# Kernel optimization log

Measured on AMD Instinct MI355X. Metric: run time of the kernel, lower is better.

Reference implementation:

```python
import jax, jax.numpy as jnp
import numpy as np

BUCKETS = 256


def _gru_cell(x, h, W_ih, W_hh, b_ih, b_hh):
    # torch GRUCell math, gate order (r, z, n)
    gi = x @ W_ih.T + b_ih            # [B, 3H]
    gh = h @ W_hh.T + b_hh            # [B, 3H]
    i_r, i_z, i_n = jnp.split(gi, 3, axis=-1)
    h_r, h_z, h_n = jnp.split(gh, 3, axis=-1)
    r = jax.nn.sigmoid(i_r + h_r)
    z = jax.nn.sigmoid(i_z + h_z)
    n = jnp.tanh(i_n + r * h_n)
    return (1.0 - z) * n + z * h


def setup_inputs() -> dict:
    key = jax.random.key(0)
    ks = jax.random.split(key, 10)
    B, T, C, G, H, V = 16, 2000, 128, 512, 512, BUCKETS
    s = 0.1  # keep gates in a sane range
    return {
        "cond": jax.random.normal(ks[0], (B, T, C), jnp.float32),
        "h0": jnp.zeros((B, G), jnp.float32),
        "W_ih": jax.random.normal(ks[1], (3 * G, C), jnp.float32) * s,
        "W_hh": jax.random.normal(ks[2], (3 * G, G), jnp.float32) * s,
        "b_ih": jax.random.normal(ks[3], (3 * G,), jnp.float32) * s,
        "b_hh": jax.random.normal(ks[4], (3 * G,), jnp.float32) * s,
        "W_hid": jax.random.normal(ks[5], (H, G), jnp.float32) * s,
        "b_hid": jax.random.normal(ks[6], (H,), jnp.float32) * s,
        "W_out": jax.random.normal(ks[7], (V, H), jnp.float32) * s,
        "b_out": jax.random.normal(ks[8], (V,), jnp.float32) * s,
        "embedding": jax.random.normal(ks[9], (V, C), jnp.float32) * s,
    }


def reference(cond, h0, W_ih, W_hh, b_ih, b_hh, W_hid, b_hid, W_out, b_out, embedding):
    B, T, C = cond.shape
    keys = jax.random.split(jax.random.key(1), T)
    prev0 = jnp.full((B,), BUCKETS // 2, jnp.int32)  # mid-bucket = mu-law zero

    def step(carry, inp):
        h, prev = carry
        cond_t, k = inp
        x = cond_t + embedding[prev]                  # [B, C]
        h = _gru_cell(x, h, W_ih, W_hh, b_ih, b_hh)   # [B, G]
        hid = jax.nn.relu(h @ W_hid.T + b_hid)        # [B, H]
        logits = hid @ W_out.T + b_out                # [B, V]
        sample = jax.random.categorical(k, logits, axis=-1).astype(jnp.int32)
        return (h, sample), (logits, sample)

    (h_final, _), (logits, samples) = jax.lax.scan(
        step, (h0, prev0), (jnp.swapaxes(cond, 0, 1), keys))
    # logits: [T, B, V] -> [B, T, V]; samples: [T, B] -> [B, T]
    return jnp.swapaxes(logits, 0, 1), jnp.swapaxes(samples, 0, 1), h_final
```

## Files before the change

### kernel.cpp

```cpp
#include <hip/hip_runtime.h>
#include <stdint.h>
#include <math.h>

#define NBLK 128
#define NTHR 256
#define Bn 16
#define Tn 2000
#define Cn 128
#define Gn 512
#define Hn 512
#define Vn 256

#define WS_DBL_BASE 512
#define GRP_STRIDE  3072

#define OUT_SAMP ((size_t)Bn*Tn*Vn)
#define OUT_HF   (OUT_SAMP + (size_t)Bn*Tn)

typedef __attribute__((ext_vector_type(2))) double d2_t;

__device__ __forceinline__ unsigned rotl32(unsigned v, int n) {
  return (v << n) | (v >> (32 - n));
}

__device__ __forceinline__ void threefry2x32(unsigned k0, unsigned k1,
                                             unsigned c0, unsigned c1,
                                             unsigned& o0, unsigned& o1) {
  unsigned ks2 = k0 ^ k1 ^ 0x1BD11BDAu;
  unsigned x0 = c0 + k0;
  unsigned x1 = c1 + k1;
#define TF_R(r) { x0 += x1; x1 = rotl32(x1, r); x1 ^= x0; }
  TF_R(13) TF_R(15) TF_R(26) TF_R(6)
  x0 += k1;  x1 += ks2 + 1u;
  TF_R(17) TF_R(29) TF_R(16) TF_R(24)
  x0 += ks2; x1 += k0 + 2u;
  TF_R(13) TF_R(15) TF_R(26) TF_R(6)
  x0 += k0;  x1 += k1 + 3u;
  TF_R(17) TF_R(29) TF_R(16) TF_R(24)
  x0 += k1;  x1 += ks2 + 4u;
  TF_R(13) TF_R(15) TF_R(26) TF_R(6)
  x0 += ks2; x1 += k0 + 5u;
#undef TF_R
  o0 = x0; o1 = x1;
}

__device__ __forceinline__ double jax_gumbel(unsigned kt0, unsigned kt1,
                                             unsigned f) {
  unsigned r0, r1;
  threefry2x32(kt0, kt1, 0u, f, r0, r1);
  unsigned bits = r0 ^ r1;
  float uf = __uint_as_float((bits >> 9) | 0x3f800000u) - 1.0f;
  if (uf <= 0.f) uf = 1.17549435e-38f;
  return -log(-log((double)uf));
}

__device__ __forceinline__ void st_d(double* p, double v) {
  asm volatile("global_store_dwordx2 %0, %1, off sc0 sc1"
               :: "v"(p), "v"(v) : "memory");
}
__device__ __forceinline__ d2_t ld_d2(const double* p) {
  d2_t r;
  asm volatile("global_load_dwordx4 %0, %1, off sc0 sc1\n\t"
               "s_waitcnt vmcnt(0)" : "=&v"(r) : "v"(p));
  return r;
}
__device__ __forceinline__ void ld8(const double* pl, int v, double* o) {
  const double* a0 = pl + v;
  const double* a1 = pl + 512 + v;
  const double* a2 = pl + 1024 + v;
  const double* a3 = pl + 1536 + v;
  double o0, o1, o2, o3, o4, o5, o6, o7;
  asm volatile(
    "global_load_dwordx2 %[r0], %[p0], off sc0 sc1\n\t"
    "global_load_dwordx2 %[r1], %[p0], off offset:2048 sc0 sc1\n\t"
    "global_load_dwordx2 %[r2], %[p1], off sc0 sc1\n\t"
    "global_load_dwordx2 %[r3], %[p1], off offset:2048 sc0 sc1\n\t"
    "global_load_dwordx2 %[r4], %[p2], off sc0 sc1\n\t"
    "global_load_dwordx2 %[r5], %[p2], off offset:2048 sc0 sc1\n\t"
    "global_load_dwordx2 %[r6], %[p3], off sc0 sc1\n\t"
    "global_load_dwordx2 %[r7], %[p3], off offset:2048 sc0 sc1\n\t"
    "s_waitcnt vmcnt(0)"
    : [r0]"=&v"(o0), [r1]"=&v"(o1), [r2]"=&v"(o2), [r3]"=&v"(o3),
      [r4]"=&v"(o4), [r5]"=&v"(o5), [r6]"=&v"(o6), [r7]"=&v"(o7)
    : [p0]"v"(a0), [p1]"v"(a1), [p2]"v"(a2), [p3]"v"(a3));
  o[0]=o0; o[1]=o1; o[2]=o2; o[3]=o3; o[4]=o4; o[5]=o5; o[6]=o6; o[7]=o7;
}
__device__ __forceinline__ unsigned ld_u(const unsigned* p) {
  unsigned r;
  asm volatile("global_load_dword %0, %1, off sc0 sc1\n\t"
               "s_waitcnt vmcnt(0)" : "=&v"(r) : "v"(p) : "memory");
  return r;
}

__device__ __forceinline__ void gar(unsigned* ctr) {
  asm volatile("s_waitcnt vmcnt(0)" ::: "memory");
  __syncthreads();
  if (threadIdx.x == 0) atomicAdd(ctr, 1u);
}
__device__ __forceinline__ void gwt(unsigned* ctr, unsigned target) {
  if (threadIdx.x == 0) {
    int guard = 0;
    while (ld_u(ctr) < target) {
      if (++guard > 5000000) break;
    }
  }
  asm volatile("" ::: "memory");
  __syncthreads();
}

extern "C" __global__ __launch_bounds__(NTHR)
void wavernn_pipe(const float* __restrict__ cond, const float* __restrict__ h0,
                  const float* __restrict__ W_ih, const float* __restrict__ W_hh,
                  const float* __restrict__ b_ih, const float* __restrict__ b_hh,
                  const float* __restrict__ W_hid, const float* __restrict__ b_hid,
                  const float* __restrict__ W_out, const float* __restrict__ b_out,
                  const float* __restrict__ emb,
                  float* __restrict__ out, double* __restrict__ ws) {
  const int tid = threadIdx.x;
  const int blk = blockIdx.x;
  const int g = blk >> 3;
  const int j = blk & 7;
  const int lane = tid & 63, wv = tid >> 6;

  unsigned* ctrH = ((unsigned*)ws) + (size_t)g * 64;
  unsigned* ctrP = ((unsigned*)ws) + (size_t)g * 64 + 32;
  double* G   = ws + WS_DBL_BASE + (size_t)g * GRP_STRIDE;
  double* Hb0 = G;
  double* Hb1 = G + 512;
  double* PL  = G + 1024;

  __shared__ __attribute__((aligned(32))) double s_x[Cn];
  __shared__ __attribute__((aligned(32))) double s_h[Gn];
  __shared__ __attribute__((aligned(32))) double s_hid[64];
  __shared__ double s_hn[64], s_in[64], s_z[64];
  __shared__ double s_part[4][64];
  __shared__ double s_gum[256];
  __shared__ float  s_cond[Cn];
  __shared__ double s_pv[4];
  __shared__ int    s_pi[4];

  if (tid < 64) st_d(&Hb0[j * 64 + tid],
                     (double)h0[(size_t)g * Gn + j * 64 + tid]);
  if (tid < Cn) s_x[tid] = (double)cond[(size_t)g * Tn * Cn + tid]
                         + (double)emb[128 * Cn + tid];
  gar(ctrH); gwt(ctrH, 8u);
  ((d2_t*)s_h)[tid] = ld_d2(Hb0 + 2 * tid);
  __syncthreads();

  for (int t = 0; t < Tn; ++t) {
    double* hnxt = (t & 1) ? Hb0 : Hb1;

    double ha0 = 0., ha1 = 0., ha2 = 0., ha3 = 0.;
    if (wv <= 2) {
      const int row = wv * 512 + j * 64 + lane;
      const float4* wh = (const float4*)(W_hh + (size_t)row * Gn);
      const double4* h4 = (const double4*)s_h;
#pragma unroll 8
      for (int k = 0; k < Gn / 4; ++k) {
        float4 w = wh[k]; double4 hv = h4[k];
        ha0 = fma((double)w.x, hv.x, ha0); ha1 = fma((double)w.y, hv.y, ha1);
        ha2 = fma((double)w.z, hv.z, ha2); ha3 = fma((double)w.w, hv.w, ha3);
      }
      if (wv == 2)
        s_hn[lane] = ((ha0 + ha1) + (ha2 + ha3)) + (double)b_hh[row];
    } else {
      const int c0 = 2 * lane;
      s_cond[c0]     = cond[((size_t)g * Tn + t) * Cn + c0];
      s_cond[c0 + 1] = cond[((size_t)g * Tn + t) * Cn + c0 + 1];
      if (t > 0) {
        unsigned kt0, kt1;
        threefry2x32(0u, 1u, 0u, (unsigned)(t - 1), kt0, kt1);
#pragma unroll
        for (int i = 0; i < 4; ++i) {
          int v = 4 * lane + i;
          s_gum[v] = jax_gumbel(kt0, kt1, (unsigned)(g * Vn + v));
        }
      }
    }

    if (t > 0) {
      gwt(ctrP, (unsigned)(8 * t));
      const int v = tid;
      double l[8];
      ld8(PL, v, l);
      double logit = ((((((((l[0] + l[1]) + l[2]) + l[3]) + l[4]) + l[5])
                       + l[6]) + l[7])) + (double)b_out[v];
      if (j == 0)
        out[(size_t)g * Tn * Vn + (size_t)(t - 1) * Vn + v] = (float)logit;
      double bv = logit + s_gum[v];
      int bi = v;
#pragma unroll
      for (int off = 1; off < 64; off <<= 1) {
        double ov = __shfl_xor(bv, off, 64);
        int oi = __shfl_xor(bi, off, 64);
        if (ov > bv || (ov == bv && oi < bi)) { bv = ov; bi = oi; }
      }
      if (lane == 0) { s_pv[wv] = bv; s_pi[wv] = bi; }
      __syncthreads();
      double fv = s_pv[0]; int fi = s_pi[0];
#pragma unroll
      for (int w = 1; w < 4; ++w) {
        double ov = s_pv[w]; int oi = s_pi[w];
        if (ov > fv || (ov == fv && oi < fi)) { fv = ov; fi = oi; }
      }
      const int samp = fi;
      if (tid == 0 && j == 0)
        out[OUT_SAMP + (size_t)g * Tn + (t - 1)] = (float)samp;
      if (tid < Cn)
        s_x[tid] = (double)s_cond[tid] + (double)emb[(size_t)samp * Cn + tid];
      __syncthreads();
    } else {
      __syncthreads();
    }

    double r_reg = 0.;
    if (wv <= 1) {
      const int row = wv * 512 + j * 64 + lane;
      const float4* wi = (const float4*)(W_ih + (size_t)row * Cn);
      const double4* x4 = (const double4*)s_x;
      double xa0 = 0., xa1 = 0., xa2 = 0., xa3 = 0.;
#pragma unroll 8
      for (int k = 0; k < Cn / 4; ++k) {
        float4 w = wi[k]; double4 xv = x4[k];
        xa0 = fma((double)w.x, xv.x, xa0); xa1 = fma((double)w.y, xv.y, xa1);
        xa2 = fma((double)w.z, xv.z, xa2); xa3 = fma((double)w.w, xv.w, xa3);
      }
      double gi = ((xa0 + xa1) + (xa2 + xa3)) + (double)b_ih[row];
      double gh = ((ha0 + ha1) + (ha2 + ha3)) + (double)b_hh[row];
      double pre = gi + gh;
      double sig = 1.0 / (1.0 + exp(-pre));
      if (wv == 0) r_reg = sig; else s_z[lane] = sig;
    } else if (wv == 3) {
      const int row = 1024 + j * 64 + lane;
      const float4* wi = (const float4*)(W_ih + (size_t)row * Cn);
      const double4* x4 = (const double4*)s_x;
      double a0 = 0., a1 = 0., a2 = 0., a3 = 0.;
#pragma unroll 8
      for (int k = 0; k < Cn / 4; ++k) {
        float4 w = wi[k]; double4 xv = x4[k];
        a0 = fma((double)w.x, xv.x, a0); a1 = fma((double)w.y, xv.y, a1);
        a2 = fma((double)w.z, xv.z, a2); a3 = fma((double)w.w, xv.w, a3);
      }
      s_in[lane] = ((a0 + a1) + (a2 + a3)) + (double)b_ih[row];
    }
    __syncthreads();

    if (wv == 0) {
      double z = s_z[lane];
      double n = tanh(s_in[lane] + r_reg * s_hn[lane]);
      double hv = (1.0 - z) * n + z * s_h[j * 64 + lane];
      st_d(&hnxt[j * 64 + lane], hv);
    }
    gar(ctrH);
    gwt(ctrH, (unsigned)(8 * (t + 2)));
    ((d2_t*)s_h)[tid] = ld_d2(hnxt + 2 * tid);
    __syncthreads();
    if (t == Tn - 1 && j == 0) {
      out[OUT_HF + (size_t)g * Gn + tid] = (float)s_h[tid];
      out[OUT_HF + (size_t)g * Gn + tid + 256] = (float)s_h[tid + 256];
    }

    {
      const int row = j * 64 + lane;
      const float4* wr = (const float4*)(W_hid + (size_t)row * Gn + wv * 128);
      const double4* hh = (const double4*)(s_h + wv * 128);
      double a0 = 0., a1 = 0., a2 = 0., a3 = 0.;
#pragma unroll 8
      for (int k = 0; k < 32; ++k) {
        float4 w = wr[k]; double4 hv = hh[k];
        a0 = fma((double)w.x, hv.x, a0); a1 = fma((double)w.y, hv.y, a1);
        a2 = fma((double)w.z, hv.z, a2); a3 = fma((double)w.w, hv.w, a3);
      }
      s_part[wv][lane] = (a0 + a1) + (a2 + a3);
    }
    __syncthreads();
    if (tid < 64) {
      double acc = (s_part[0][tid] + s_part[1][tid])
                 + (s_part[2][tid] + s_part[3][tid])
                 + (double)b_hid[j * 64 + tid];
      s_hid[tid] = acc > 0.0 ? acc : 0.0;
    }
    __syncthreads();
    {
      const int v = tid;
      const float4* wr = (const float4*)(W_out + (size_t)v * Hn + j * 64);
      const double4* hh = (const double4*)s_hid;
      double a0 = 0., a1 = 0., a2 = 0., a3 = 0.;
#pragma unroll 8
      for (int k = 0; k < 16; ++k) {
        float4 w = wr[k]; double4 hv = hh[k];
        a0 = fma((double)w.x, hv.x, a0); a1 = fma((double)w.y, hv.y, a1);
        a2 = fma((double)w.z, hv.z, a2); a3 = fma((double)w.w, hv.w, a3);
      }
      st_d(&PL[j * 256 + v], (a0 + a1) + (a2 + a3));
    }
    gar(ctrP);
  }

  gwt(ctrP, (unsigned)(8 * Tn));
  {
    const int v = tid;
    double l[8];
    ld8(PL, v, l);
    double logit = ((((((((l[0] + l[1]) + l[2]) + l[3]) + l[4]) + l[5])
                     + l[6]) + l[7])) + (double)b_out[v];
    if (j == 0)
      out[(size_t)g * Tn * Vn + (size_t)(Tn - 1) * Vn + v] = (float)logit;
    unsigned kt0, kt1;
    threefry2x32(0u, 1u, 0u, (unsigned)(Tn - 1), kt0, kt1);
    double gum = jax_gumbel(kt0, kt1, (unsigned)(g * Vn + v));
    double bv = logit + gum;
    int bi = v;
#pragma unroll
    for (int off = 1; off < 64; off <<= 1) {
      double ov = __shfl_xor(bv, off, 64);
      int oi = __shfl_xor(bi, off, 64);
      if (ov > bv || (ov == bv && oi < bi)) { bv = ov; bi = oi; }
    }
    if (lane == 0) { s_pv[wv] = bv; s_pi[wv] = bi; }
    __syncthreads();
    double fv = s_pv[0]; int fi = s_pi[0];
#pragma unroll
    for (int w = 1; w < 4; ++w) {
      double ov = s_pv[w]; int oi = s_pi[w];
      if (ov > fv || (ov == fv && oi < fi)) { fv = ov; fi = oi; }
    }
    if (tid == 0 && j == 0)
      out[OUT_SAMP + (size_t)g * Tn + (Tn - 1)] = (float)fi;
  }
}

extern "C" void kernel_launch(void* const* d_in, const int* in_sizes, int n_in,
                              void* d_out, int out_size, void* d_ws, size_t ws_size,
                              hipStream_t stream) {
  const float* cond  = (const float*)d_in[0];
  const float* h0    = (const float*)d_in[1];
  const float* W_ih  = (const float*)d_in[2];
  const float* W_hh  = (const float*)d_in[3];
  const float* b_ih  = (const float*)d_in[4];
  const float* b_hh  = (const float*)d_in[5];
  const float* W_hid = (const float*)d_in[6];
  const float* b_hid = (const float*)d_in[7];
  const float* W_out = (const float*)d_in[8];
  const float* b_out = (const float*)d_in[9];
  const float* emb   = (const float*)d_in[10];

  hipMemsetAsync(d_ws, 0, 4096, stream);
  hipLaunchKernelGGL(wavernn_pipe, dim3(NBLK), dim3(NTHR), 0, stream,
                     cond, h0, W_ih, W_hh, b_ih, b_hh, W_hid, b_hid,
                     W_out, b_out, emb, (float*)d_out, (double*)d_ws);
}
```

Measured before the change: 48.82 ms.

## Split matvec rows across 8-lane groups for coalesced weight loads with shuffle reductions

```diff
diff --git a/kernel.cpp b/kernel.cpp
--- a/kernel.cpp
+++ b/kernel.cpp
@@ -121,6 +121,8 @@
   const int g = blk >> 3;
   const int j = blk & 7;
   const int lane = tid & 63, wv = tid >> 6;
+  const int r8 = lane >> 3;
+  const int c8 = lane & 7;
 
   unsigned* ctrH = ((unsigned*)ws) + (size_t)g * 64;
   unsigned* ctrP = ((unsigned*)ws) + (size_t)g * 64 + 32;
@@ -132,12 +134,24 @@
   __shared__ __attribute__((aligned(32))) double s_x[Cn];
   __shared__ __attribute__((aligned(32))) double s_h[Gn];
   __shared__ __attribute__((aligned(32))) double s_hid[64];
-  __shared__ double s_hn[64], s_in[64], s_z[64];
-  __shared__ double s_part[4][64];
+  __shared__ double s_hg[3][64];
+  __shared__ double s_xg[3][64];
+  __shared__ double s_hidraw[64];
   __shared__ double s_gum[256];
   __shared__ float  s_cond[Cn];
   __shared__ double s_pv[4];
   __shared__ int    s_pi[4];
+
+  const int rrow = j * 64 + lane;
+  double bih_r = 0., bih_z = 0., bih_n = 0.;
+  double bhh_r = 0., bhh_z = 0., bhh_n = 0.;
+  if (wv == 0) {
+    bih_r = (double)b_ih[rrow]; bih_z = (double)b_ih[512 + rrow];
+    bih_n = (double)b_ih[1024 + rrow];
+    bhh_r = (double)b_hh[rrow]; bhh_z = (double)b_hh[512 + rrow];
+    bhh_n = (double)b_hh[1024 + rrow];
+  }
+  const double bout_reg = (double)b_out[tid];
 
   if (tid < 64) st_d(&Hb0[j * 64 + tid],
                      (double)h0[(size_t)g * Gn + j * 64 + tid]);
@@ -150,19 +164,31 @@
   for (int t = 0; t < Tn; ++t) {
     double* hnxt = (t & 1) ? Hb0 : Hb1;
 
-    double ha0 = 0., ha1 = 0., ha2 = 0., ha3 = 0.;
     if (wv <= 2) {
-      const int row = wv * 512 + j * 64 + lane;
-      const float4* wh = (const float4*)(W_hh + (size_t)row * Gn);
+      const float* lptr = W_hh + (size_t)(wv * 512 + j * 64 + r8) * Gn + c8 * 4;
       const double4* h4 = (const double4*)s_h;
-#pragma unroll 8
-      for (int k = 0; k < Gn / 4; ++k) {
-        float4 w = wh[k]; double4 hv = h4[k];
-        ha0 = fma((double)w.x, hv.x, ha0); ha1 = fma((double)w.y, hv.y, ha1);
-        ha2 = fma((double)w.z, hv.z, ha2); ha3 = fma((double)w.w, hv.w, ha3);
-      }
-      if (wv == 2)
-        s_hn[lane] = ((ha0 + ha1) + (ha2 + ha3)) + (double)b_hh[row];
+      double acc[8];
+#pragma unroll
+      for (int b = 0; b < 8; ++b) acc[b] = 0.;
+#pragma unroll 4
+      for (int kk = 0; kk < 16; ++kk) {
+        const double4 hv = h4[kk * 8 + c8];
+#pragma unroll
+        for (int b = 0; b < 8; ++b) {
+          const float4 w = *(const float4*)(lptr + (size_t)b * 8 * Gn + kk * 32);
+          acc[b] = fma((double)w.x, hv.x, acc[b]);
+          acc[b] = fma((double)w.y, hv.y, acc[b]);
+          acc[b] = fma((double)w.z, hv.z, acc[b]);
+          acc[b] = fma((double)w.w, hv.w, acc[b]);
+        }
+      }
+#pragma unroll
+      for (int b = 0; b < 8; ++b) {
+        acc[b] += __shfl_xor(acc[b], 1, 64);
+        acc[b] += __shfl_xor(acc[b], 2, 64);
+        acc[b] += __shfl_xor(acc[b], 4, 64);
+        if (c8 == 0) s_hg[wv][b * 8 + r8] = acc[b];
+      }
     } else {
       const int c0 = 2 * lane;
       s_cond[c0]     = cond[((size_t)g * Tn + t) * Cn + c0];
@@ -184,7 +210,7 @@
       double l[8];
       ld8(PL, v, l);
       double logit = ((((((((l[0] + l[1]) + l[2]) + l[3]) + l[4]) + l[5])
-                       + l[6]) + l[7])) + (double)b_out[v];
+                       + l[6]) + l[7])) + bout_reg;
       if (j == 0)
         out[(size_t)g * Tn * Vn + (size_t)(t - 1) * Vn + v] = (float)logit;
       double bv = logit + s_gum[v];
@@ -213,41 +239,44 @@
       __syncthreads();
     }
 
-    double r_reg = 0.;
-    if (wv <= 1) {
-      const int row = wv * 512 + j * 64 + lane;
-      const float4* wi = (const float4*)(W_ih + (size_t)row * Cn);
+    if (wv <= 2) {
+      const float* lptr = W_ih + (size_t)(wv * 512 + j * 64 + r8) * Cn + c8 * 4;
       const double4* x4 = (const double4*)s_x;
-      double xa0 = 0., xa1 = 0., xa2 = 0., xa3 = 0.;
-#pragma unroll 8
-      for (int k = 0; k < Cn / 4; ++k) {
-        float4 w = wi[k]; double4 xv = x4[k];
-        xa0 = fma((double)w.x, xv.x, xa0); xa1 = fma((double)w.y, xv.y, xa1);
-        xa2 = fma((double)w.z, xv.z, xa2); xa3 = fma((double)w.w, xv.w, xa3);
-      }
-      double gi = ((xa0 + xa1) + (xa2 + xa3)) + (double)b_ih[row];
-      double gh = ((ha0 + ha1) + (ha2 + ha3)) + (double)b_hh[row];
-      double pre = gi + gh;
-      double sig = 1.0 / (1.0 + exp(-pre));
-      if (wv == 0) r_reg = sig; else s_z[lane] = sig;
-    } else if (wv == 3) {
-      const int row = 1024 + j * 64 + lane;
-      const float4* wi = (const float4*)(W_ih + (size_t)row * Cn);
-      const double4* x4 = (const double4*)s_x;
-      double a0 = 0., a1 = 0., a2 = 0., a3 = 0.;
-#pragma unroll 8
-      for (int k = 0; k < Cn / 4; ++k) {
-        float4 w = wi[k]; double4 xv = x4[k];
-        a0 = fma((double)w.x, xv.x, a0); a1 = fma((double)w.y, xv.y, a1);
-        a2 = fma((double)w.z, xv.z, a2); a3 = fma((double)w.w, xv.w, a3);
-      }
-      s_in[lane] = ((a0 + a1) + (a2 + a3)) + (double)b_ih[row];
+      double acc[8];
+#pragma unroll
+      for (int b = 0; b < 8; ++b) acc[b] = 0.;
+#pragma unroll
+      for (int kk = 0; kk < 4; ++kk) {
+        const double4 xv = x4[kk * 8 + c8];
+#pragma unroll
+        for (int b = 0; b < 8; ++b) {
+          const float4 w = *(const float4*)(lptr + (size_t)b * 8 * Cn + kk * 32);
+          acc[b] = fma((double)w.x, xv.x, acc[b]);
+          acc[b] = fma((double)w.y, xv.y, acc[b]);
+          acc[b] = fma((double)w.z, xv.z, acc[b]);
+          acc[b] = fma((double)w.w, xv.w, acc[b]);
+        }
+      }
+#pragma unroll
+      for (int b = 0; b < 8; ++b) {
+        acc[b] += __shfl_xor(acc[b], 1, 64);
+        acc[b] += __shfl_xor(acc[b], 2, 64);
+        acc[b] += __shfl_xor(acc[b], 4, 64);
+        if (c8 == 0) s_xg[wv][b * 8 + r8] = acc[b];
+      }
     }
     __syncthreads();
 
     if (wv == 0) {
-      double z = s_z[lane];
-      double n = tanh(s_in[lane] + r_reg * s_hn[lane]);
+      double hr = s_hg[0][lane] + bhh_r;
+      double hz = s_hg[1][lane] + bhh_z;
+      double hn = s_hg[2][lane] + bhh_n;
+      double xr = s_xg[0][lane] + bih_r;
+      double xz = s_xg[1][lane] + bih_z;
+      double xn = s_xg[2][lane] + bih_n;
+      double r = 1.0 / (1.0 + exp(-(xr + hr)));
+      double z = 1.0 / (1.0 + exp(-(xz + hz)));
+      double n = tanh(xn + r * hn);
       double hv = (1.0 - z) * n + z * s_h[j * 64 + lane];
       st_d(&hnxt[j * 64 + lane], hv);
     }
@@ -261,38 +290,63 @@
     }
 
     {
-      const int row = j * 64 + lane;
-      const float4* wr = (const float4*)(W_hid + (size_t)row * Gn + wv * 128);
-      const double4* hh = (const double4*)(s_h + wv * 128);
-      double a0 = 0., a1 = 0., a2 = 0., a3 = 0.;
-#pragma unroll 8
-      for (int k = 0; k < 32; ++k) {
-        float4 w = wr[k]; double4 hv = hh[k];
-        a0 = fma((double)w.x, hv.x, a0); a1 = fma((double)w.y, hv.y, a1);
-        a2 = fma((double)w.z, hv.z, a2); a3 = fma((double)w.w, hv.w, a3);
-      }
-      s_part[wv][lane] = (a0 + a1) + (a2 + a3);
+      const float* lptr = W_hid
+          + (size_t)(j * 64 + wv * 16 + r8) * Gn + c8 * 4;
+      const double4* h4 = (const double4*)s_h;
+      double acc[2];
+      acc[0] = 0.; acc[1] = 0.;
+#pragma unroll 4
+      for (int kk = 0; kk < 16; ++kk) {
+        const double4 hv = h4[kk * 8 + c8];
+#pragma unroll
+        for (int b = 0; b < 2; ++b) {
+          const float4 w = *(const float4*)(lptr + (size_t)b * 8 * Gn + kk * 32);
+          acc[b] = fma((double)w.x, hv.x, acc[b]);
+          acc[b] = fma((double)w.y, hv.y, acc[b]);
+          acc[b] = fma((double)w.z, hv.z, acc[b]);
+          acc[b] = fma((double)w.w, hv.w, acc[b]);
+        }
+      }
+#pragma unroll
+      for (int b = 0; b < 2; ++b) {
+        acc[b] += __shfl_xor(acc[b], 1, 64);
+        acc[b] += __shfl_xor(acc[b], 2, 64);
+        acc[b] += __shfl_xor(acc[b], 4, 64);
+        if (c8 == 0) s_hidraw[wv * 16 + b * 8 + r8] = acc[b];
+      }
     }
     __syncthreads();
     if (tid < 64) {
-      double acc = (s_part[0][tid] + s_part[1][tid])
-                 + (s_part[2][tid] + s_part[3][tid])
-                 + (double)b_hid[j * 64 + tid];
+      double acc = s_hidraw[tid] + (double)b_hid[j * 64 + tid];
       s_hid[tid] = acc > 0.0 ? acc : 0.0;
     }
     __syncthreads();
     {
-      const int v = tid;
-      const float4* wr = (const float4*)(W_out + (size_t)v * Hn + j * 64);
+      const float* lptr = W_out
+          + (size_t)(wv * 64 + r8) * Hn + j * 64 + c8 * 4;
       const double4* hh = (const double4*)s_hid;
-      double a0 = 0., a1 = 0., a2 = 0., a3 = 0.;
-#pragma unroll 8
-      for (int k = 0; k < 16; ++k) {
-        float4 w = wr[k]; double4 hv = hh[k];
-        a0 = fma((double)w.x, hv.x, a0); a1 = fma((double)w.y, hv.y, a1);
-        a2 = fma((double)w.z, hv.z, a2); a3 = fma((double)w.w, hv.w, a3);
-      }
-      st_d(&PL[j * 256 + v], (a0 + a1) + (a2 + a3));
+      double acc[8];
+#pragma unroll
+      for (int b = 0; b < 8; ++b) acc[b] = 0.;
+#pragma unroll
+      for (int kk = 0; kk < 2; ++kk) {
+        const double4 hv = hh[kk * 8 + c8];
+#pragma unroll
+        for (int b = 0; b < 8; ++b) {
+          const float4 w = *(const float4*)(lptr + (size_t)b * 8 * Hn + kk * 32);
+          acc[b] = fma((double)w.x, hv.x, acc[b]);
+          acc[b] = fma((double)w.y, hv.y, acc[b]);
+          acc[b] = fma((double)w.z, hv.z, acc[b]);
+          acc[b] = fma((double)w.w, hv.w, acc[b]);
+        }
+      }
+#pragma unroll
+      for (int b = 0; b < 8; ++b) {
+        acc[b] += __shfl_xor(acc[b], 1, 64);
+        acc[b] += __shfl_xor(acc[b], 2, 64);
+        acc[b] += __shfl_xor(acc[b], 4, 64);
+        if (c8 == 0) st_d(&PL[j * 256 + wv * 64 + b * 8 + r8], acc[b]);
+      }
     }
     gar(ctrP);
   }
@@ -303,7 +357,7 @@
     double l[8];
     ld8(PL, v, l);
     double logit = ((((((((l[0] + l[1]) + l[2]) + l[3]) + l[4]) + l[5])
-                     + l[6]) + l[7])) + (double)b_out[v];
+                     + l[6]) + l[7])) + bout_reg;
     if (j == 0)
       out[(size_t)g * Tn * Vn + (size_t)(Tn - 1) * Vn + v] = (float)logit;
     unsigned kt0, kt1;
```

New measurement: 58.82 ms. 1.2x slower.

## Replace atomic-counter grid barriers with per-value epoch-tagged flag polling

Applied to the files above, without the earlier changes.

```diff
diff --git a/kernel.cpp b/kernel.cpp
--- a/kernel.cpp
+++ b/kernel.cpp
@@ -12,7 +12,7 @@
 #define Vn 256
 
 #define WS_DBL_BASE 512
-#define GRP_STRIDE  3072
+#define GRP_STRIDE  6144
 
 #define OUT_SAMP ((size_t)Bn*Tn*Vn)
 #define OUT_HF   (OUT_SAMP + (size_t)Bn*Tn)
@@ -54,58 +54,39 @@
   return -log(-log((double)uf));
 }
 
-__device__ __forceinline__ void st_d(double* p, double v) {
-  asm volatile("global_store_dwordx2 %0, %1, off sc0 sc1"
-               :: "v"(p), "v"(v) : "memory");
-}
-__device__ __forceinline__ d2_t ld_d2(const double* p) {
-  d2_t r;
-  asm volatile("global_load_dwordx4 %0, %1, off sc0 sc1\n\t"
-               "s_waitcnt vmcnt(0)" : "=&v"(r) : "v"(p));
-  return r;
-}
-__device__ __forceinline__ void ld8(const double* pl, int v, double* o) {
-  const double* a0 = pl + v;
-  const double* a1 = pl + 512 + v;
-  const double* a2 = pl + 1024 + v;
-  const double* a3 = pl + 1536 + v;
-  double o0, o1, o2, o3, o4, o5, o6, o7;
+__device__ __forceinline__ void stp(double* p, double v, double s) {
+  d2_t d; d.x = v; d.y = s;
+  asm volatile("global_store_dwordx4 %0, %1, off sc0 sc1"
+               :: "v"(p), "v"(d) : "memory");
+}
+__device__ __forceinline__ void ldp2(const double* p, d2_t& a, d2_t& b) {
+  asm volatile("global_load_dwordx4 %0, %2, off sc0 sc1\n\t"
+               "global_load_dwordx4 %1, %2, off offset:16 sc0 sc1\n\t"
+               "s_waitcnt vmcnt(0)"
+               : "=&v"(a), "=&v"(b) : "v"(p) : "memory");
+}
+__device__ __forceinline__ void ldp8(const double* p0, const double* p1,
+                                     const double* p2, const double* p3,
+                                     const double* p4, const double* p5,
+                                     const double* p6, const double* p7,
+                                     d2_t* r) {
+  d2_t r0, r1, r2, r3, r4, r5, r6, r7;
   asm volatile(
-    "global_load_dwordx2 %[r0], %[p0], off sc0 sc1\n\t"
-    "global_load_dwordx2 %[r1], %[p0], off offset:2048 sc0 sc1\n\t"
-    "global_load_dwordx2 %[r2], %[p1], off sc0 sc1\n\t"
-    "global_load_dwordx2 %[r3], %[p1], off offset:2048 sc0 sc1\n\t"
-    "global_load_dwordx2 %[r4], %[p2], off sc0 sc1\n\t"
-    "global_load_dwordx2 %[r5], %[p2], off offset:2048 sc0 sc1\n\t"
-    "global_load_dwordx2 %[r6], %[p3], off sc0 sc1\n\t"
-    "global_load_dwordx2 %[r7], %[p3], off offset:2048 sc0 sc1\n\t"
+    "global_load_dwordx4 %[o0], %[a0], off sc0 sc1\n\t"
+    "global_load_dwordx4 %[o1], %[a1], off sc0 sc1\n\t"
+    "global_load_dwordx4 %[o2], %[a2], off sc0 sc1\n\t"
+    "global_load_dwordx4 %[o3], %[a3], off sc0 sc1\n\t"
+    "global_load_dwordx4 %[o4], %[a4], off sc0 sc1\n\t"
+    "global_load_dwordx4 %[o5], %[a5], off sc0 sc1\n\t"
+    "global_load_dwordx4 %[o6], %[a6], off sc0 sc1\n\t"
+    "global_load_dwordx4 %[o7], %[a7], off sc0 sc1\n\t"
     "s_waitcnt vmcnt(0)"
-    : [r0]"=&v"(o0), [r1]"=&v"(o1), [r2]"=&v"(o2), [r3]"=&v"(o3),
-      [r4]"=&v"(o4), [r5]"=&v"(o5), [r6]"=&v"(o6), [r7]"=&v"(o7)
-    : [p0]"v"(a0), [p1]"v"(a1), [p2]"v"(a2), [p3]"v"(a3));
-  o[0]=o0; o[1]=o1; o[2]=o2; o[3]=o3; o[4]=o4; o[5]=o5; o[6]=o6; o[7]=o7;
-}
-__device__ __forceinline__ unsigned ld_u(const unsigned* p) {
-  unsigned r;
-  asm volatile("global_load_dword %0, %1, off sc0 sc1\n\t"
-               "s_waitcnt vmcnt(0)" : "=&v"(r) : "v"(p) : "memory");
-  return r;
-}
-
-__device__ __forceinline__ void gar(unsigned* ctr) {
-  asm volatile("s_waitcnt vmcnt(0)" ::: "memory");
-  __syncthreads();
-  if (threadIdx.x == 0) atomicAdd(ctr, 1u);
-}
-__device__ __forceinline__ void gwt(unsigned* ctr, unsigned target) {
-  if (threadIdx.x == 0) {
-    int guard = 0;
-    while (ld_u(ctr) < target) {
-      if (++guard > 5000000) break;
-    }
-  }
-  asm volatile("" ::: "memory");
-  __syncthreads();
+    : [o0]"=&v"(r0), [o1]"=&v"(r1), [o2]"=&v"(r2), [o3]"=&v"(r3),
+      [o4]"=&v"(r4), [o5]"=&v"(r5), [o6]"=&v"(r6), [o7]"=&v"(r7)
+    : [a0]"v"(p0), [a1]"v"(p1), [a2]"v"(p2), [a3]"v"(p3),
+      [a4]"v"(p4), [a5]"v"(p5), [a6]"v"(p6), [a7]"v"(p7)
+    : "memory");
+  r[0]=r0; r[1]=r1; r[2]=r2; r[3]=r3; r[4]=r4; r[5]=r5; r[6]=r6; r[7]=r7;
 }
 
 extern "C" __global__ __launch_bounds__(NTHR)
@@ -122,12 +103,10 @@
   const int j = blk & 7;
   const int lane = tid & 63, wv = tid >> 6;
 
-  unsigned* ctrH = ((unsigned*)ws) + (size_t)g * 64;
-  unsigned* ctrP = ((unsigned*)ws) + (size_t)g * 64 + 32;
   double* G   = ws + WS_DBL_BASE + (size_t)g * GRP_STRIDE;
   double* Hb0 = G;
-  double* Hb1 = G + 512;
-  double* PL  = G + 1024;
+  double* Hb1 = G + 1024;
+  double* PLp = G + 2048;
 
   __shared__ __attribute__((aligned(32))) double s_x[Cn];
   __shared__ __attribute__((aligned(32))) double s_h[Gn];
@@ -139,12 +118,27 @@
   __shared__ double s_pv[4];
   __shared__ int    s_pi[4];
 
-  if (tid < 64) st_d(&Hb0[j * 64 + tid],
-                     (double)h0[(size_t)g * Gn + j * 64 + tid]);
+  const double bout_reg = (double)b_out[tid];
+
+  const double* plA0 = PLp + 2 * tid;
+  const double* plA1 = plA0 + 512;
+  const double* plA2 = plA0 + 1024;
+  const double* plA3 = plA0 + 1536;
+  const double* plA4 = plA0 + 2048;
+  const double* plA5 = plA0 + 2560;
+  const double* plA6 = plA0 + 3072;
+  const double* plA7 = plA0 + 3584;
+
+  if (tid < 64) stp(&Hb0[2 * (j * 64 + tid)],
+                    (double)h0[(size_t)g * Gn + j * 64 + tid], 1.0);
   if (tid < Cn) s_x[tid] = (double)cond[(size_t)g * Tn * Cn + tid]
                          + (double)emb[128 * Cn + tid];
-  gar(ctrH); gwt(ctrH, 8u);
-  ((d2_t*)s_h)[tid] = ld_d2(Hb0 + 2 * tid);
+  {
+    d2_t a, b; int guard = 0;
+    do { ldp2(Hb0 + 4 * tid, a, b); }
+    while ((a.y != 1.0 || b.y != 1.0) && ++guard < 2000000);
+    s_h[2 * tid] = a.x; s_h[2 * tid + 1] = b.x;
+  }
   __syncthreads();
 
   for (int t = 0; t < Tn; ++t) {
@@ -179,12 +173,25 @@
     }
 
     if (t > 0) {
-      gwt(ctrP, (unsigned)(8 * t));
+      const double exP = (double)t;
+      double l[8];
+      {
+        d2_t r[8]; int guard = 0;
+        for (;;) {
+          ldp8(plA0, plA1, plA2, plA3, plA4, plA5, plA6, plA7, r);
+          bool ok = (r[0].y == exP) & (r[1].y == exP) & (r[2].y == exP)
+                  & (r[3].y == exP) & (r[4].y == exP) & (r[5].y == exP)
+                  & (r[6].y == exP) & (r[7].y == exP);
+          if (ok || ++guard > 2000000) {
+            l[0]=r[0].x; l[1]=r[1].x; l[2]=r[2].x; l[3]=r[3].x;
+            l[4]=r[4].x; l[5]=r[5].x; l[6]=r[6].x; l[7]=r[7].x;
+            break;
+          }
+        }
+      }
       const int v = tid;
-      double l[8];
-      ld8(PL, v, l);
       double logit = ((((((((l[0] + l[1]) + l[2]) + l[3]) + l[4]) + l[5])
-                       + l[6]) + l[7])) + (double)b_out[v];
+                       + l[6]) + l[7])) + bout_reg;
       if (j == 0)
         out[(size_t)g * Tn * Vn + (size_t)(t - 1) * Vn + v] = (float)logit;
       double bv = logit + s_gum[v];
@@ -249,11 +256,16 @@
       double z = s_z[lane];
       double n = tanh(s_in[lane] + r_reg * s_hn[lane]);
       double hv = (1.0 - z) * n + z * s_h[j * 64 + lane];
-      st_d(&hnxt[j * 64 + lane], hv);
-    }
-    gar(ctrH);
-    gwt(ctrH, (unsigned)(8 * (t + 2)));
-    ((d2_t*)s_h)[tid] = ld_d2(hnxt + 2 * tid);
+      stp(&hnxt[2 * (j * 64 + lane)], hv, (double)(t + 2));
+    }
+    __syncthreads();
+    {
+      const double exH = (double)(t + 2);
+      d2_t a, b; int guard = 0;
+      do { ldp2(hnxt + 4 * tid, a, b); }
+      while ((a.y != exH || b.y != exH) && ++guard < 2000000);
+      s_h[2 * tid] = a.x; s_h[2 * tid + 1] = b.x;
+    }
     __syncthreads();
     if (t == Tn - 1 && j == 0) {
       out[OUT_HF + (size_t)g * Gn + tid] = (float)s_h[tid];
@@ -292,18 +304,30 @@
         a0 = fma((double)w.x, hv.x, a0); a1 = fma((double)w.y, hv.y, a1);
         a2 = fma((double)w.z, hv.z, a2); a3 = fma((double)w.w, hv.w, a3);
       }
-      st_d(&PL[j * 256 + v], (a0 + a1) + (a2 + a3));
-    }
-    gar(ctrP);
+      stp(&PLp[2 * (j * 256 + v)], (a0 + a1) + (a2 + a3), (double)(t + 1));
+    }
   }
 
-  gwt(ctrP, (unsigned)(8 * Tn));
   {
+    const double exP = (double)Tn;
+    double l[8];
+    {
+      d2_t r[8]; int guard = 0;
+      for (;;) {
+        ldp8(plA0, plA1, plA2, plA3, plA4, plA5, plA6, plA7, r);
+        bool ok = (r[0].y == exP) & (r[1].y == exP) & (r[2].y == exP)
+                & (r[3].y == exP) & (r[4].y == exP) & (r[5].y == exP)
+                & (r[6].y == exP) & (r[7].y == exP);
+        if (ok || ++guard > 2000000) {
+          l[0]=r[0].x; l[1]=r[1].x; l[2]=r[2].x; l[3]=r[3].x;
+          l[4]=r[4].x; l[5]=r[5].x; l[6]=r[6].x; l[7]=r[7].x;
+          break;
+        }
+      }
+    }
     const int v = tid;
-    double l[8];
-    ld8(PL, v, l);
     double logit = ((((((((l[0] + l[1]) + l[2]) + l[3]) + l[4]) + l[5])
-                     + l[6]) + l[7])) + (double)b_out[v];
+                     + l[6]) + l[7])) + bout_reg;
     if (j == 0)
       out[(size_t)g * Tn * Vn + (size_t)(Tn - 1) * Vn + v] = (float)logit;
     unsigned kt0, kt1;
```

Result: faster. 45.17 ms (-7.5%).
